# Kernel tuning notes

Hardware: AMD Instinct MI355X
Metric: run time of the kernel (lower is better)

Reference implementation:

```python
import jax, jax.numpy as jnp
import numpy as np

EPS = 1e-5

def _ln(x, g, b):
    m = jnp.mean(x, axis=-1, keepdims=True)
    v = jnp.var(x, axis=-1, keepdims=True)
    return (x - m) / jnp.sqrt(v + EPS) * g + b

def _lin(x, w, b):
    # torch-style weight [out, in]
    return x @ w.T + b

def _mlp(x, w1, b1, w2, b2):
    # Mlp: Linear -> exact GELU -> Linear (dropout=0)
    return _lin(jax.nn.gelu(_lin(x, w1, b1), approximate=False), w2, b2)

def setup_inputs() -> dict:
    B, C, H, W = 2, 256, 64, 64
    key = jax.random.key(0)
    ks = jax.random.split(key, 32)
    s = 0.02  # param init scale keeps attention logits in a sane range
    d = {
        'center_fea': jax.random.normal(ks[0], (B, C, H, W), jnp.float32),
        'wh_fea':     jax.random.normal(ks[1], (B, C, H, W), jnp.float32),
        'cls_fea':    jax.random.normal(ks[2], (B, C, H, W), jnp.float32),
        'mix_w': jax.random.normal(ks[3], (C, 3 * C), jnp.float32) * s,
        'mix_b': jnp.zeros((C,), jnp.float32),
        'ln_g': jnp.ones((C,), jnp.float32),
        'ln_b': jnp.zeros((C,), jnp.float32),
        'q1_w': jax.random.normal(ks[4], (C, C), jnp.float32) * s,
        'q1_b': jnp.zeros((C,), jnp.float32),
        'q2_w': jax.random.normal(ks[5], (C, C), jnp.float32) * s,
        'q2_b': jnp.zeros((C,), jnp.float32),
        'q3_w': jax.random.normal(ks[6], (C, C), jnp.float32) * s,
        'q3_b': jnp.zeros((C,), jnp.float32),
        'k_w': jax.random.normal(ks[7], (C, C), jnp.float32) * s,
        'k_b': jnp.zeros((C,), jnp.float32),
        'v_w': jax.random.normal(ks[8], (C, C), jnp.float32) * s,
        'v_b': jnp.zeros((C,), jnp.float32),
        'cmlp_w1': jax.random.normal(ks[9], (C, C), jnp.float32) * s,
        'cmlp_b1': jnp.zeros((C,), jnp.float32),
        'cmlp_w2': jax.random.normal(ks[10], (C, C), jnp.float32) * s,
        'cmlp_b2': jnp.zeros((C,), jnp.float32),
        'wmlp_w1': jax.random.normal(ks[11], (C, C), jnp.float32) * s,
        'wmlp_b1': jnp.zeros((C,), jnp.float32),
        'wmlp_w2': jax.random.normal(ks[12], (C, C), jnp.float32) * s,
        'wmlp_b2': jnp.zeros((C,), jnp.float32),
        'clsmlp_w1': jax.random.normal(ks[13], (C, C), jnp.float32) * s,
        'clsmlp_b1': jnp.zeros((C,), jnp.float32),
        'clsmlp_w2': jax.random.normal(ks[14], (C, C), jnp.float32) * s,
        'clsmlp_b2': jnp.zeros((C,), jnp.float32),
    }
    return d

def reference(center_fea, wh_fea, cls_fea, mix_w, mix_b, ln_g, ln_b,
              q1_w, q1_b, q2_w, q2_b, q3_w, q3_b, k_w, k_b, v_w, v_b,
              cmlp_w1, cmlp_b1, cmlp_w2, cmlp_b2,
              wmlp_w1, wmlp_b1, wmlp_w2, wmlp_b2,
              clsmlp_w1, clsmlp_b1, clsmlp_w2, clsmlp_b2):
    b, c, h, w = center_fea.shape
    # 1x1 conv mix over concatenated channels [b, 3c, h, w] -> [b, c, h, w]
    cat = jnp.concatenate([center_fea, wh_fea, cls_fea], axis=1)
    mix = jnp.einsum('oc,bchw->bohw', mix_w, cat) + mix_b[None, :, None, None]

    tok = lambda x: x.reshape(b, c, h * w).transpose(0, 2, 1)  # [b, N, c]
    cf, wf, clf, mf = tok(center_fea), tok(wh_fea), tok(cls_fea), tok(mix)

    ct, wt, clt, mt = _ln(cf, ln_g, ln_b), _ln(wf, ln_g, ln_b), _ln(clf, ln_g, ln_b), _ln(mf, ln_g, ln_b)

    kf = _lin(mt, k_w, k_b)  # shared K
    vf = _lin(mt, v_w, v_b)  # shared V

    def attend(q):
        score = jax.nn.softmax(jnp.einsum('bnd,bmd->bnm', q, kf), axis=-1)  # [b, N, N]
        return jnp.einsum('bnm,bmd->bnd', score, vf)

    cf  = _ln(cf  + attend(_lin(ct,  q1_w, q1_b)), ln_g, ln_b)
    wf  = _ln(wf  + attend(_lin(wt,  q2_w, q2_b)), ln_g, ln_b)
    clf = _ln(clf + attend(_lin(clt, q3_w, q3_b)), ln_g, ln_b)

    cf  = _ln(cf  + _mlp(cf,  cmlp_w1, cmlp_b1, cmlp_w2, cmlp_b2), ln_g, ln_b)
    wf  = _ln(wf  + _mlp(wf,  wmlp_w1, wmlp_b1, wmlp_w2, wmlp_b2), ln_g, ln_b)
    clf = _ln(clf + _mlp(clf, clsmlp_w1, clsmlp_b1, clsmlp_w2, clsmlp_b2), ln_g, ln_b)

    untok = lambda x: x.transpose(0, 2, 1).reshape(b, c, h, w)
    return (untok(cf), untok(wf), untok(clf))
```

## Files before the change

kernel.cpp:

```cpp
#include <hip/hip_runtime.h>
#include <hip/hip_bf16.h>
#include <math.h>

typedef unsigned int   u32;
typedef unsigned short u16;
typedef float floatx4 __attribute__((ext_vector_type(4)));
typedef short bf16x8  __attribute__((ext_vector_type(8)));

#define MFMA16(a,b,c) __builtin_amdgcn_mfma_f32_16x16x32_bf16((a),(b),(c),0,0,0)

static __device__ __forceinline__ float bfbits2f(u16 h){
    return __uint_as_float(((u32)h) << 16);
}
static __device__ __forceinline__ u16 f2bfbits(float f){
    u32 u = __float_as_uint(f);
    u32 r = (u + 0x7fffu + ((u >> 16) & 1u)) >> 16;
    return (u16)r;
}
static __device__ __forceinline__ bool sniff_bf16(const void* ln_g){
    return ((const u32*)ln_g)[0] == 0x3f803f80u;
}

typedef __attribute__((address_space(1))) const unsigned int gas_u32;
typedef __attribute__((address_space(3))) unsigned int las_u32;
static __device__ __forceinline__ void gl_lds16(const void* g, void* l){
    __builtin_amdgcn_global_load_lds((gas_u32*)g, (las_u32*)l, 16, 0, 0);
}

#define DPPF(v, ctrl) __uint_as_float((u32)__builtin_amdgcn_update_dpp( \
        (int)__float_as_uint(v), (int)__float_as_uint(v), (ctrl), 0xf, 0xf, true))

static __device__ __forceinline__ float red16_max(float v){
    v = fmaxf(v, DPPF(v, 0xB1));
    v = fmaxf(v, DPPF(v, 0x4E));
    v = fmaxf(v, DPPF(v, 0x141));
    v = fmaxf(v, DPPF(v, 0x140));
    return v;
}
static __device__ __forceinline__ float red16_sum(float v){
    v += DPPF(v, 0xB1);
    v += DPPF(v, 0x4E);
    v += DPPF(v, 0x141);
    v += DPPF(v, 0x140);
    return v;
}

struct PackJob { const void* src; void* dst; int n; int mode; };
struct PackParams { PackJob jobs[26]; const void* lng; };

__global__ __launch_bounds__(256) void k_pack(PackParams p){
    bool isb = sniff_bf16(p.lng);
    PackJob j = p.jobs[blockIdx.y];
    for (int i = blockIdx.x * 256 + threadIdx.x; i < j.n; i += 256 * 256){
        float v = isb ? bfbits2f(((const u16*)j.src)[i]) : ((const float*)j.src)[i];
        if (j.mode == 0) ((u16*)j.dst)[i]  = f2bfbits(v);
        else             ((float*)j.dst)[i] = v;
    }
}

struct FtParams { const void* src[3]; u16* dst[3]; const void* lng; };

__global__ __launch_bounds__(256) void k_feat_t(FtParams p){
    bool isb = sniff_bf16(p.lng);
    int z = blockIdx.z; int si = z >> 1; int b = z & 1;
    const void* src = p.src[si]; u16* dst = p.dst[si];
    int n0 = blockIdx.x * 64, c0 = blockIdx.y * 64;
    __shared__ float tile[64][65];
    int t = threadIdx.x; int tx = t & 63; int ty = t >> 6;
    #pragma unroll
    for (int pp = 0; pp < 16; ++pp){
        int cl = ty + pp * 4;
        size_t off = ((size_t)b * 256 + c0 + cl) * 4096 + n0 + tx;
        float v = isb ? bfbits2f(((const u16*)src)[off]) : ((const float*)src)[off];
        tile[cl][tx] = v;
    }
    __syncthreads();
    #pragma unroll
    for (int pp = 0; pp < 16; ++pp){
        int nl = ty + pp * 4; int cl = tx;
        dst[((size_t)b * 4096 + n0 + nl) * 256 + c0 + cl] = f2bfbits(tile[cl][nl]);
    }
}

struct GemmJob { const u16* A0; const u16* A1; const u16* A2;
                 const u16* W; const float* bias; const u16* res; u16* out; };
struct GemmParams { GemmJob jobs[5]; int K; int op; };

__global__ __launch_bounds__(256, 4) void k_gemm(GemmParams p){
    GemmJob j = p.jobs[blockIdx.z];
    int m0 = blockIdx.x * 64, n0 = blockIdx.y * 64;
    __shared__ __align__(16) u16 As[2][64][64];
    __shared__ __align__(16) u16 Bs[2][64][64];
    int t = threadIdx.x;
    int wave = t >> 6, lane = t & 63, l15 = lane & 15, quad = lane >> 4;
    int mh = (wave & 1) * 32, nh = (wave >> 1) * 32;
    int key = l15 & 7;

    auto stage = [&](int bi, int k0){
        const u16* Ap = (k0 < 256) ? j.A0 : (k0 < 512 ? j.A1 : j.A2);
        int koff = k0 & 255;
        #pragma unroll
        for (int i = 0; i < 2; ++i){
            int rq = wave * 2 + i;
            int r  = rq * 8 + (lane >> 3);
            int gs = (lane & 7) ^ (r & 7);
            gl_lds16(Ap  + (size_t)(m0 + r) * 256 + koff + gs * 8, &As[bi][rq * 8][0]);
            gl_lds16(j.W + (size_t)(n0 + r) * p.K + k0   + gs * 8, &Bs[bi][rq * 8][0]);
        }
    };

    floatx4 acc[2][2];
    #pragma unroll
    for (int a = 0; a < 2; ++a)
        #pragma unroll
        for (int bq = 0; bq < 2; ++bq) acc[a][bq] = (floatx4){0.f,0.f,0.f,0.f};

    stage(0, 0);
    __syncthreads();
    int nk = p.K >> 6, buf = 0;

    for (int ks = 0; ks < nk; ++ks){
        if (ks + 1 < nk) stage(buf ^ 1, (ks + 1) * 64);
        #pragma unroll
        for (int kc = 0; kc < 2; ++kc){
            int gsel = ((kc * 4 + quad) ^ key) * 8;
            bf16x8 a0 = *(const bf16x8*)&As[buf][mh +      l15][gsel];
            bf16x8 a1 = *(const bf16x8*)&As[buf][mh + 16 + l15][gsel];
            bf16x8 b0 = *(const bf16x8*)&Bs[buf][nh +      l15][gsel];
            bf16x8 b1 = *(const bf16x8*)&Bs[buf][nh + 16 + l15][gsel];
            acc[0][0] = MFMA16(a0, b0, acc[0][0]);
            acc[0][1] = MFMA16(a0, b1, acc[0][1]);
            acc[1][0] = MFMA16(a1, b0, acc[1][0]);
            acc[1][1] = MFMA16(a1, b1, acc[1][1]);
        }
        __syncthreads();
        buf ^= 1;
    }

    #pragma unroll
    for (int mb = 0; mb < 2; ++mb)
        #pragma unroll
        for (int nb = 0; nb < 2; ++nb){
            int col = n0 + nh + nb * 16 + l15;
            float bias = j.bias[col];
            #pragma unroll
            for (int rg = 0; rg < 4; ++rg){
                int row = m0 + mh + mb * 16 + quad * 4 + rg;
                float v = acc[mb][nb][rg] + bias;
                if (p.op == 1)      v = 0.5f * v * (1.0f + erff(v * 0.70710678118f));
                else if (p.op == 2) v += bfbits2f(j.res[(size_t)row * 256 + col]);
                j.out[(size_t)row * 256 + col] = f2bfbits(v);
            }
        }
}

struct LnJob { const u16* src; u16* dst; };
struct LnParams { LnJob jobs[4]; const float* g; const float* b; };

__global__ __launch_bounds__(256, 4) void k_ln(LnParams p){
    LnJob j = p.jobs[blockIdx.y];
    int g16 = threadIdx.x >> 4, l = threadIdx.x & 15;
    size_t tok = (size_t)blockIdx.x * 16 + g16;
    const u16* row = j.src + tok * 256 + l * 16;
    uint4 ra = *(const uint4*)(row);
    uint4 rb = *(const uint4*)(row + 8);
    u32 wv[8] = {ra.x, ra.y, ra.z, ra.w, rb.x, rb.y, rb.z, rb.w};
    float va[16];
    float s1 = 0.f, s2 = 0.f;
    #pragma unroll
    for (int i = 0; i < 8; ++i){
        float a = bfbits2f((u16)(wv[i] & 0xffffu));
        float c = bfbits2f((u16)(wv[i] >> 16));
        va[2*i] = a; va[2*i+1] = c;
        s1 += a + c; s2 += a*a + c*c;
    }
    s1 = red16_sum(s1); s2 = red16_sum(s2);
    float mean = s1 * (1.f/256.f);
    float var  = s2 * (1.f/256.f) - mean * mean;
    float rstd = rsqrtf(var + 1e-5f);
    int c0 = l * 16;
    u32 ow[8];
    #pragma unroll
    for (int i = 0; i < 8; ++i){
        float x0 = (va[2*i]   - mean) * rstd * p.g[c0 + 2*i]     + p.b[c0 + 2*i];
        float x1 = (va[2*i+1] - mean) * rstd * p.g[c0 + 2*i + 1] + p.b[c0 + 2*i + 1];
        ow[i] = (u32)f2bfbits(x0) | ((u32)f2bfbits(x1) << 16);
    }
    u16* dst = j.dst + tok * 256 + c0;
    *(uint4*)(dst)     = (uint4){ow[0], ow[1], ow[2], ow[3]};
    *(uint4*)(dst + 8) = (uint4){ow[4], ow[5], ow[6], ow[7]};
}

__global__ __launch_bounds__(256, 4) void k_vt(const u16* __restrict__ Vf, u16* __restrict__ Vt){
    int b = blockIdx.z;
    int n0 = blockIdx.x * 64, c0 = blockIdx.y * 64;
    __shared__ u16 tile[64][66];
    int t = threadIdx.x; int tx = t & 63; int ty = t >> 6;
    #pragma unroll
    for (int pp = 0; pp < 16; ++pp){
        int nl = ty + pp * 4;
        tile[nl][tx] = Vf[((size_t)b * 4096 + n0 + nl) * 256 + c0 + tx];
    }
    __syncthreads();
    #pragma unroll
    for (int pp = 0; pp < 16; ++pp){
        int cl = ty + pp * 4; int nl = tx;
        Vt[((size_t)b * 256 + c0 + cl) * 4096 + n0 + nl] = tile[nl][cl];
    }
}

struct FlashParams {
    const u16* Q[3]; const u16* K; const u16* Vt;
    const u16* Res[3]; u16* Out[3];
    const float* g; const float* b;
};

__global__ __launch_bounds__(256, 2) void k_flash(FlashParams p){
    int s = blockIdx.y >> 1, b = blockIdx.y & 1;
    int m0 = blockIdx.x * 64;
    const u16* Q   = p.Q[s]   + (size_t)b * 4096 * 256;
    const u16* Kf  = p.K      + (size_t)b * 4096 * 256;
    const u16* Vtg = p.Vt     + (size_t)b * 256 * 4096;
    const u16* Res = p.Res[s] + (size_t)b * 4096 * 256;
    u16*       Out = p.Out[s] + (size_t)b * 4096 * 256;

    __shared__ __align__(16) u16 Kb[2][32][256];
    __shared__ __align__(16) u16 Vb[2][256][32];
    __shared__ __align__(16) u16 Pl[4][16][40];

    int t = threadIdx.x, wave = t >> 6, lane = t & 63, l15 = lane & 15, quad = lane >> 4;

    auto stage = [&](int bi, int kv0){
        #pragma unroll
        for (int m = 0; m < 4; ++m){
            int q = wave * 4 + m;
            int r0 = q * 2 + (lane >> 5);
            int gg = (lane & 31) ^ (r0 & 7);
            gl_lds16(Kf + (size_t)(kv0 + r0) * 256 + gg * 8, &Kb[bi][q * 2][0]);
        }
        #pragma unroll
        for (int m = 0; m < 4; ++m){
            int q = wave * 4 + m;
            int d = q * 16 + (lane >> 2);
            int gg = (lane & 3) ^ ((d >> 1) & 3);
            gl_lds16(Vtg + (size_t)d * 4096 + kv0 + gg * 8, &Vb[bi][q * 16][0]);
        }
    };

    stage(0, 0);

    bf16x8 qf[8];
    {
        const u16* qrow = Q + (size_t)(m0 + wave * 16 + l15) * 256 + quad * 8;
        #pragma unroll
        for (int kc = 0; kc < 8; ++kc) qf[kc] = *(const bf16x8*)(qrow + kc * 32);
    }
    floatx4 o[16];
    #pragma unroll
    for (int i = 0; i < 16; ++i) o[i] = (floatx4){0.f,0.f,0.f,0.f};
    float mrow[4] = {-INFINITY,-INFINITY,-INFINITY,-INFINITY};
    float lsum[4] = {0.f,0.f,0.f,0.f};

    __syncthreads();
    int buf = 0;

    for (int ch = 0; ch < 128; ++ch){
        if (ch < 127) stage(buf ^ 1, (ch + 1) * 32);

        floatx4 sa[2];
        __builtin_amdgcn_s_setprio(1);
        #pragma unroll
        for (int sub = 0; sub < 2; ++sub){
            int row = sub * 16 + l15;
            floatx4 a0 = (floatx4){0.f,0.f,0.f,0.f};
            floatx4 a1 = (floatx4){0.f,0.f,0.f,0.f};
            #pragma unroll
            for (int kc = 0; kc < 4; ++kc){
                bf16x8 kb0 = *(const bf16x8*)&Kb[buf][row][((((2*kc  ) * 4 + quad) ^ (row & 7))) * 8];
                bf16x8 kb1 = *(const bf16x8*)&Kb[buf][row][((((2*kc+1) * 4 + quad) ^ (row & 7))) * 8];
                a0 = MFMA16(qf[2*kc  ], kb0, a0);
                a1 = MFMA16(qf[2*kc+1], kb1, a1);
            }
            sa[sub] = a0 + a1;
        }
        __builtin_amdgcn_s_setprio(0);

        float al[4]; int grow = 0;
        #pragma unroll
        for (int rg = 0; rg < 4; ++rg){
            float m1 = red16_max(fmaxf(sa[0][rg], sa[1][rg]));
            grow |= (m1 > mrow[rg]) ? 1 : 0;
            float mn = fmaxf(mrow[rg], m1);
            al[rg] = __expf(mrow[rg] - mn);
            mrow[rg] = mn;
        }
        #pragma unroll
        for (int rg = 0; rg < 4; ++rg){
            float p0 = __expf(sa[0][rg] - mrow[rg]);
            float p1 = __expf(sa[1][rg] - mrow[rg]);
            sa[0][rg] = p0; sa[1][rg] = p1;
            lsum[rg] = lsum[rg] * al[rg] + (p0 + p1);
        }

        #pragma unroll
        for (int sub = 0; sub < 2; ++sub)
            #pragma unroll
            for (int rg = 0; rg < 4; ++rg)
                Pl[wave][quad * 4 + rg][sub * 16 + l15] = f2bfbits(sa[sub][rg]);

        if (__any(grow)){
            #pragma unroll
            for (int dc = 0; dc < 16; ++dc)
                #pragma unroll
                for (int rg = 0; rg < 4; ++rg) o[dc][rg] *= al[rg];
        }

        asm volatile("s_waitcnt lgkmcnt(0)" ::: "memory");
        __builtin_amdgcn_sched_barrier(0);

        bf16x8 pa = *(const bf16x8*)&Pl[wave][l15][quad * 8];
        __builtin_amdgcn_s_setprio(1);
        #pragma unroll
        for (int dc = 0; dc < 16; ++dc){
            int row = dc * 16 + l15;
            bf16x8 vb = *(const bf16x8*)&Vb[buf][row][((quad ^ ((row >> 1) & 3))) * 8];
            o[dc] = MFMA16(pa, vb, o[dc]);
        }
        __builtin_amdgcn_s_setprio(0);

        __syncthreads();
        buf ^= 1;
    }

    float inv[4];
    #pragma unroll
    for (int rg = 0; rg < 4; ++rg) inv[rg] = 1.0f / red16_sum(lsum[rg]);
    float s1[4] = {0.f,0.f,0.f,0.f}, s2[4] = {0.f,0.f,0.f,0.f};
    #pragma unroll
    for (int dc = 0; dc < 16; ++dc)
        #pragma unroll
        for (int rg = 0; rg < 4; ++rg){
            int row = m0 + wave * 16 + quad * 4 + rg;
            float v = o[dc][rg] * inv[rg] + bfbits2f(Res[(size_t)row * 256 + dc * 16 + l15]);
            o[dc][rg] = v;
            s1[rg] += v; s2[rg] += v * v;
        }
    #pragma unroll
    for (int rg = 0; rg < 4; ++rg){
        float mean = red16_sum(s1[rg]) * (1.f/256.f);
        float q2   = red16_sum(s2[rg]);
        float var  = q2 * (1.f/256.f) - mean * mean;
        s1[rg] = mean; s2[rg] = rsqrtf(var + 1e-5f);
    }
    #pragma unroll
    for (int dc = 0; dc < 16; ++dc){
        int c = dc * 16 + l15;
        float gv = p.g[c], bv = p.b[c];
        #pragma unroll
        for (int rg = 0; rg < 4; ++rg){
            int row = m0 + wave * 16 + quad * 4 + rg;
            Out[(size_t)row * 256 + c] = f2bfbits((o[dc][rg] - s1[rg]) * s2[rg] * gv + bv);
        }
    }
}

struct OutTParams { const u16* F[3]; void* out; const void* lng; };

__global__ __launch_bounds__(256, 4) void k_out_t(OutTParams p){
    bool isb = sniff_bf16(p.lng);
    int z = blockIdx.z; int s = z >> 1; int b = z & 1;
    const u16* F = p.F[s];
    int n0 = blockIdx.x * 64, c0 = blockIdx.y * 64;
    __shared__ u16 tile[64][66];
    int t = threadIdx.x; int tx = t & 63; int ty = t >> 6;
    #pragma unroll
    for (int pp = 0; pp < 16; ++pp){
        int nl = ty + pp * 4;
        tile[nl][tx] = F[((size_t)b * 4096 + n0 + nl) * 256 + c0 + tx];
    }
    __syncthreads();
    size_t obase = ((size_t)s * 2 + b) * 256 * 4096;
    #pragma unroll
    for (int pp = 0; pp < 16; ++pp){
        int cl = ty + pp * 4; int nl = tx;
        u16 raw = tile[nl][cl];
        size_t off = obase + (size_t)(c0 + cl) * 4096 + n0 + nl;
        if (isb) ((u16*)p.out)[off]   = raw;
        else     ((float*)p.out)[off] = bfbits2f(raw);
    }
}

extern "C" void kernel_launch(void* const* d_in, const int* in_sizes, int n_in,
                              void* d_out, int out_size, void* d_ws, size_t ws_size,
                              hipStream_t stream) {
    (void)in_sizes; (void)n_in; (void)out_size; (void)ws_size;
    const size_t SLOT = (size_t)2 * 4096 * 256;
    u16* ws = (u16*)d_ws;
    auto slot = [&](int i){ return ws + (size_t)i * SLOT; };

    u16 *Tc = slot(0),  *Tw = slot(1),  *Tcl = slot(2),  *Tm = slot(3);
    u16 *Lc = slot(4),  *Lw = slot(5),  *Lcl = slot(6),  *Lm = slot(7);
    u16 *Q1 = slot(8),  *Q2 = slot(9),  *Q3  = slot(10);
    u16 *Kf = slot(11), *Vf = slot(12), *Vt  = slot(13);
    u16 *Yc = slot(14), *Yw = slot(15), *Ycl = slot(16);
    u16 *Hc = Q1, *Hw = Q2, *Hcl = Q3;
    u16 *Zc = Lc, *Zw = Lw, *Zcl = Lcl;
    u16 *Fc = Kf, *Fw = Vf, *Fcl = Vt;

    u16* wbase = slot(17);
    u16 *mixw = wbase;
    u16 *q1w = wbase + 196608, *q2w = q1w + 65536, *q3w = q2w + 65536;
    u16 *kw  = q3w + 65536,    *vw  = kw  + 65536;
    u16 *cw1 = vw  + 65536, *cw2 = cw1 + 65536, *ww1 = cw2 + 65536,
        *ww2 = ww1 + 65536, *clw1 = ww2 + 65536, *clw2 = clw1 + 65536;
    float* pbase = (float*)(wbase + 1048576);
    float *mixb = pbase,        *lng = pbase+256,  *lnb = pbase+512,
          *q1b = pbase+768,  *q2b = pbase+1024, *q3b = pbase+1280,
          *kb  = pbase+1536, *vb  = pbase+1792,
          *cb1 = pbase+2048, *cb2 = pbase+2304, *wb1 = pbase+2560,
          *wb2 = pbase+2816, *clb1= pbase+3072, *clb2= pbase+3328;

    {
        PackParams pp;
        const int widx[12] = {3,7,9,11,13,15,17,19,21,23,25,27};
        u16* wdst[12] = {mixw,q1w,q2w,q3w,kw,vw,cw1,cw2,ww1,ww2,clw1,clw2};
        for (int i = 0; i < 12; ++i)
            pp.jobs[i] = PackJob{ d_in[widx[i]], wdst[i], (i==0?196608:65536), 0 };
        const int pidx[14] = {4,5,6,8,10,12,14,16,18,20,22,24,26,28};
        float* pdst[14] = {mixb,lng,lnb,q1b,q2b,q3b,kb,vb,cb1,cb2,wb1,wb2,clb1,clb2};
        for (int i = 0; i < 14; ++i)
            pp.jobs[12+i] = PackJob{ d_in[pidx[i]], pdst[i], 256, 1 };
        pp.lng = d_in[5];
        hipLaunchKernelGGL(k_pack, dim3(256, 26), dim3(256), 0, stream, pp);
    }
    {
        FtParams fp;
        fp.src[0] = d_in[0]; fp.src[1] = d_in[1]; fp.src[2] = d_in[2];
        fp.dst[0] = Tc; fp.dst[1] = Tw; fp.dst[2] = Tcl;
        fp.lng = d_in[5];
        hipLaunchKernelGGL(k_feat_t, dim3(64, 4, 6), dim3(256), 0, stream, fp);
    }
    {
        GemmParams gp; gp.K = 768; gp.op = 0;
        gp.jobs[0] = GemmJob{ Tc, Tw, Tcl, mixw, mixb, nullptr, Tm };
        hipLaunchKernelGGL(k_gemm, dim3(128, 4, 1), dim3(256), 0, stream, gp);
    }
    {
        LnParams lp; lp.g = lng; lp.b = lnb;
        lp.jobs[0] = LnJob{Tc, Lc}; lp.jobs[1] = LnJob{Tw, Lw};
        lp.jobs[2] = LnJob{Tcl, Lcl}; lp.jobs[3] = LnJob{Tm, Lm};
        hipLaunchKernelGGL(k_ln, dim3(512, 4), dim3(256), 0, stream, lp);
    }
    {
        GemmParams gp; gp.K = 256; gp.op = 0;
        gp.jobs[0] = GemmJob{ Lc,  nullptr, nullptr, q1w, q1b, nullptr, Q1 };
        gp.jobs[1] = GemmJob{ Lw,  nullptr, nullptr, q2w, q2b, nullptr, Q2 };
        gp.jobs[2] = GemmJob{ Lcl, nullptr, nullptr, q3w, q3b, nullptr, Q3 };
        gp.jobs[3] = GemmJob{ Lm,  nullptr, nullptr, kw,  kb,  nullptr, Kf };
        gp.jobs[4] = GemmJob{ Lm,  nullptr, nullptr, vw,  vb,  nullptr, Vf };
        hipLaunchKernelGGL(k_gemm, dim3(128, 4, 5), dim3(256), 0, stream, gp);
    }
    hipLaunchKernelGGL(k_vt, dim3(64, 4, 2), dim3(256), 0, stream, Vf, Vt);
    {
        FlashParams fp;
        fp.Q[0] = Q1; fp.Q[1] = Q2; fp.Q[2] = Q3;
        fp.K = Kf; fp.Vt = Vt;
        fp.Res[0] = Tc; fp.Res[1] = Tw; fp.Res[2] = Tcl;
        fp.Out[0] = Yc; fp.Out[1] = Yw; fp.Out[2] = Ycl;
        fp.g = lng; fp.b = lnb;
        hipLaunchKernelGGL(k_flash, dim3(64, 6), dim3(256), 0, stream, fp);
    }
    {
        GemmParams gp; gp.K = 256; gp.op = 1;
        gp.jobs[0] = GemmJob{ Yc,  nullptr, nullptr, cw1,  cb1,  nullptr, Hc };
        gp.jobs[1] = GemmJob{ Yw,  nullptr, nullptr, ww1,  wb1,  nullptr, Hw };
        gp.jobs[2] = GemmJob{ Ycl, nullptr, nullptr, clw1, clb1, nullptr, Hcl };
        hipLaunchKernelGGL(k_gemm, dim3(128, 4, 3), dim3(256), 0, stream, gp);
    }
    {
        GemmParams gp; gp.K = 256; gp.op = 2;
        gp.jobs[0] = GemmJob{ Hc,  nullptr, nullptr, cw2,  cb2,  Yc,  Zc };
        gp.jobs[1] = GemmJob{ Hw,  nullptr, nullptr, ww2,  wb2,  Yw,  Zw };
        gp.jobs[2] = GemmJob{ Hcl, nullptr, nullptr, clw2, clb2, Ycl, Zcl };
        hipLaunchKernelGGL(k_gemm, dim3(128, 4, 3), dim3(256), 0, stream, gp);
    }
    {
        LnParams lp; lp.g = lng; lp.b = lnb;
        lp.jobs[0] = LnJob{Zc, Fc}; lp.jobs[1] = LnJob{Zw, Fw};
        lp.jobs[2] = LnJob{Zcl, Fcl}; lp.jobs[3] = LnJob{Zc, Fc};
        hipLaunchKernelGGL(k_ln, dim3(512, 3), dim3(256), 0, stream, lp);
    }
    {
        OutTParams op;
        op.F[0] = Fc; op.F[1] = Fw; op.F[2] = Fcl;
        op.out = d_out; op.lng = d_in[5];
        hipLaunchKernelGGL(k_out_t, dim3(64, 4, 6), dim3(256), 0, stream, op);
    }
}
```

Measured before the change: 426.2 us.

## Fuse final LayerNorm with output transpose, template GEMM on BM, drop setprio

```diff
diff --git a/kernel.cpp b/kernel.cpp
--- a/kernel.cpp
+++ b/kernel.cpp
@@ -86,32 +86,42 @@
                  const u16* W; const float* bias; const u16* res; u16* out; };
 struct GemmParams { GemmJob jobs[5]; int K; int op; };
 
-__global__ __launch_bounds__(256, 4) void k_gemm(GemmParams p){
+template<int BM>
+__global__ __launch_bounds__(256, (BM == 64) ? 4 : 3) void k_gemm(GemmParams p){
+    constexpr int MW = BM / 2;
+    constexpr int MB = MW / 16;
+    constexpr int AI = BM / 32;
     GemmJob j = p.jobs[blockIdx.z];
-    int m0 = blockIdx.x * 64, n0 = blockIdx.y * 64;
-    __shared__ __align__(16) u16 As[2][64][64];
+    int m0 = blockIdx.x * BM, n0 = blockIdx.y * 64;
+    __shared__ __align__(16) u16 As[2][BM][64];
     __shared__ __align__(16) u16 Bs[2][64][64];
     int t = threadIdx.x;
     int wave = t >> 6, lane = t & 63, l15 = lane & 15, quad = lane >> 4;
-    int mh = (wave & 1) * 32, nh = (wave >> 1) * 32;
+    int mh = (wave & 1) * MW, nh = (wave >> 1) * 32;
     int key = l15 & 7;
 
     auto stage = [&](int bi, int k0){
         const u16* Ap = (k0 < 256) ? j.A0 : (k0 < 512 ? j.A1 : j.A2);
         int koff = k0 & 255;
+        #pragma unroll
+        for (int i = 0; i < AI; ++i){
+            int rq = wave * AI + i;
+            int r  = rq * 8 + (lane >> 3);
+            int gs = (lane & 7) ^ (r & 7);
+            gl_lds16(Ap + (size_t)(m0 + r) * 256 + koff + gs * 8, &As[bi][rq * 8][0]);
+        }
         #pragma unroll
         for (int i = 0; i < 2; ++i){
             int rq = wave * 2 + i;
             int r  = rq * 8 + (lane >> 3);
             int gs = (lane & 7) ^ (r & 7);
-            gl_lds16(Ap  + (size_t)(m0 + r) * 256 + koff + gs * 8, &As[bi][rq * 8][0]);
-            gl_lds16(j.W + (size_t)(n0 + r) * p.K + k0   + gs * 8, &Bs[bi][rq * 8][0]);
+            gl_lds16(j.W + (size_t)(n0 + r) * p.K + k0 + gs * 8, &Bs[bi][rq * 8][0]);
         }
     };
 
-    floatx4 acc[2][2];
-    #pragma unroll
-    for (int a = 0; a < 2; ++a)
+    floatx4 acc[MB][2];
+    #pragma unroll
+    for (int a = 0; a < MB; ++a)
         #pragma unroll
         for (int bq = 0; bq < 2; ++bq) acc[a][bq] = (floatx4){0.f,0.f,0.f,0.f};
 
@@ -124,21 +134,24 @@
         #pragma unroll
         for (int kc = 0; kc < 2; ++kc){
             int gsel = ((kc * 4 + quad) ^ key) * 8;
-            bf16x8 a0 = *(const bf16x8*)&As[buf][mh +      l15][gsel];
-            bf16x8 a1 = *(const bf16x8*)&As[buf][mh + 16 + l15][gsel];
-            bf16x8 b0 = *(const bf16x8*)&Bs[buf][nh +      l15][gsel];
-            bf16x8 b1 = *(const bf16x8*)&Bs[buf][nh + 16 + l15][gsel];
-            acc[0][0] = MFMA16(a0, b0, acc[0][0]);
-            acc[0][1] = MFMA16(a0, b1, acc[0][1]);
-            acc[1][0] = MFMA16(a1, b0, acc[1][0]);
-            acc[1][1] = MFMA16(a1, b1, acc[1][1]);
+            bf16x8 av[MB], bv[2];
+            #pragma unroll
+            for (int mb = 0; mb < MB; ++mb)
+                av[mb] = *(const bf16x8*)&As[buf][mh + mb * 16 + l15][gsel];
+            bv[0] = *(const bf16x8*)&Bs[buf][nh +      l15][gsel];
+            bv[1] = *(const bf16x8*)&Bs[buf][nh + 16 + l15][gsel];
+            #pragma unroll
+            for (int mb = 0; mb < MB; ++mb){
+                acc[mb][0] = MFMA16(av[mb], bv[0], acc[mb][0]);
+                acc[mb][1] = MFMA16(av[mb], bv[1], acc[mb][1]);
+            }
         }
         __syncthreads();
         buf ^= 1;
     }
 
     #pragma unroll
-    for (int mb = 0; mb < 2; ++mb)
+    for (int mb = 0; mb < MB; ++mb)
         #pragma unroll
         for (int nb = 0; nb < 2; ++nb){
             int col = n0 + nh + nb * 16 + l15;
@@ -191,6 +204,57 @@
     *(uint4*)(dst + 8) = (uint4){ow[4], ow[5], ow[6], ow[7]};
 }
 
+struct LnOutParams { const u16* Z[3]; void* out; const float* g; const float* b; const void* lng; };
+
+__global__ __launch_bounds__(256, 4) void k_ln_out(LnOutParams p){
+    bool isb = sniff_bf16(p.lng);
+    int y = blockIdx.y; int s = y >> 1, b = y & 1;
+    const u16* Z = p.Z[s] + (size_t)b * 4096 * 256;
+    int tok0 = blockIdx.x * 64;
+    __shared__ u16 tile[64][258];
+    int t = threadIdx.x, g16 = t >> 4, l = t & 15;
+    #pragma unroll
+    for (int pass = 0; pass < 4; ++pass){
+        int tl = pass * 16 + g16;
+        const u16* row = Z + (size_t)(tok0 + tl) * 256 + l * 16;
+        uint4 ra = *(const uint4*)(row);
+        uint4 rb = *(const uint4*)(row + 8);
+        u32 wv[8] = {ra.x, ra.y, ra.z, ra.w, rb.x, rb.y, rb.z, rb.w};
+        float va[16];
+        float s1 = 0.f, s2 = 0.f;
+        #pragma unroll
+        for (int i = 0; i < 8; ++i){
+            float a = bfbits2f((u16)(wv[i] & 0xffffu));
+            float c = bfbits2f((u16)(wv[i] >> 16));
+            va[2*i] = a; va[2*i+1] = c;
+            s1 += a + c; s2 += a*a + c*c;
+        }
+        s1 = red16_sum(s1); s2 = red16_sum(s2);
+        float mean = s1 * (1.f/256.f);
+        float var  = s2 * (1.f/256.f) - mean * mean;
+        float rstd = rsqrtf(var + 1e-5f);
+        int c0 = l * 16;
+        u32* drow = (u32*)&tile[tl][c0];
+        #pragma unroll
+        for (int i = 0; i < 8; ++i){
+            float x0 = (va[2*i]   - mean) * rstd * p.g[c0 + 2*i]     + p.b[c0 + 2*i];
+            float x1 = (va[2*i+1] - mean) * rstd * p.g[c0 + 2*i + 1] + p.b[c0 + 2*i + 1];
+            drow[i] = (u32)f2bfbits(x0) | ((u32)f2bfbits(x1) << 16);
+        }
+    }
+    __syncthreads();
+    size_t obase = ((size_t)s * 2 + b) * 256 * 4096;
+    int cq = t >> 6, tl2 = t & 63;
+    #pragma unroll
+    for (int pp = 0; pp < 64; ++pp){
+        int c = pp * 4 + cq;
+        u16 raw = tile[tl2][c];
+        size_t off = obase + (size_t)c * 4096 + tok0 + tl2;
+        if (isb) ((u16*)p.out)[off]   = raw;
+        else     ((float*)p.out)[off] = bfbits2f(raw);
+    }
+}
+
 __global__ __launch_bounds__(256, 4) void k_vt(const u16* __restrict__ Vf, u16* __restrict__ Vt){
     int b = blockIdx.z;
     int n0 = blockIdx.x * 64, c0 = blockIdx.y * 64;
@@ -268,7 +332,6 @@
         if (ch < 127) stage(buf ^ 1, (ch + 1) * 32);
 
         floatx4 sa[2];
-        __builtin_amdgcn_s_setprio(1);
         #pragma unroll
         for (int sub = 0; sub < 2; ++sub){
             int row = sub * 16 + l15;
@@ -283,7 +346,6 @@
             }
             sa[sub] = a0 + a1;
         }
-        __builtin_amdgcn_s_setprio(0);
 
         float al[4]; int grow = 0;
         #pragma unroll
@@ -319,14 +381,12 @@
         __builtin_amdgcn_sched_barrier(0);
 
         bf16x8 pa = *(const bf16x8*)&Pl[wave][l15][quad * 8];
-        __builtin_amdgcn_s_setprio(1);
         #pragma unroll
         for (int dc = 0; dc < 16; ++dc){
             int row = dc * 16 + l15;
             bf16x8 vb = *(const bf16x8*)&Vb[buf][row][((quad ^ ((row >> 1) & 3))) * 8];
             o[dc] = MFMA16(pa, vb, o[dc]);
         }
-        __builtin_amdgcn_s_setprio(0);
 
         __syncthreads();
         buf ^= 1;
@@ -361,32 +421,6 @@
             int row = m0 + wave * 16 + quad * 4 + rg;
             Out[(size_t)row * 256 + c] = f2bfbits((o[dc][rg] - s1[rg]) * s2[rg] * gv + bv);
         }
-    }
-}
-
-struct OutTParams { const u16* F[3]; void* out; const void* lng; };
-
-__global__ __launch_bounds__(256, 4) void k_out_t(OutTParams p){
-    bool isb = sniff_bf16(p.lng);
-    int z = blockIdx.z; int s = z >> 1; int b = z & 1;
-    const u16* F = p.F[s];
-    int n0 = blockIdx.x * 64, c0 = blockIdx.y * 64;
-    __shared__ u16 tile[64][66];
-    int t = threadIdx.x; int tx = t & 63; int ty = t >> 6;
-    #pragma unroll
-    for (int pp = 0; pp < 16; ++pp){
-        int nl = ty + pp * 4;
-        tile[nl][tx] = F[((size_t)b * 4096 + n0 + nl) * 256 + c0 + tx];
-    }
-    __syncthreads();
-    size_t obase = ((size_t)s * 2 + b) * 256 * 4096;
-    #pragma unroll
-    for (int pp = 0; pp < 16; ++pp){
-        int cl = ty + pp * 4; int nl = tx;
-        u16 raw = tile[nl][cl];
-        size_t off = obase + (size_t)(c0 + cl) * 4096 + n0 + nl;
-        if (isb) ((u16*)p.out)[off]   = raw;
-        else     ((float*)p.out)[off] = bfbits2f(raw);
     }
 }
 
@@ -405,7 +439,6 @@
     u16 *Yc = slot(14), *Yw = slot(15), *Ycl = slot(16);
     u16 *Hc = Q1, *Hw = Q2, *Hcl = Q3;
     u16 *Zc = Lc, *Zw = Lw, *Zcl = Lcl;
-    u16 *Fc = Kf, *Fw = Vf, *Fcl = Vt;
 
     u16* wbase = slot(17);
     u16 *mixw = wbase;
@@ -443,7 +476,7 @@
     {
         GemmParams gp; gp.K = 768; gp.op = 0;
         gp.jobs[0] = GemmJob{ Tc, Tw, Tcl, mixw, mixb, nullptr, Tm };
-        hipLaunchKernelGGL(k_gemm, dim3(128, 4, 1), dim3(256), 0, stream, gp);
+        hipLaunchKernelGGL((k_gemm<64>), dim3(128, 4, 1), dim3(256), 0, stream, gp);
     }
     {
         LnParams lp; lp.g = lng; lp.b = lnb;
@@ -458,7 +491,7 @@
         gp.jobs[2] = GemmJob{ Lcl, nullptr, nullptr, q3w, q3b, nullptr, Q3 };
         gp.jobs[3] = GemmJob{ Lm,  nullptr, nullptr, kw,  kb,  nullptr, Kf };
         gp.jobs[4] = GemmJob{ Lm,  nullptr, nullptr, vw,  vb,  nullptr, Vf };
-        hipLaunchKernelGGL(k_gemm, dim3(128, 4, 5), dim3(256), 0, stream, gp);
+        hipLaunchKernelGGL((k_gemm<128>), dim3(64, 4, 5), dim3(256), 0, stream, gp);
     }
     hipLaunchKernelGGL(k_vt, dim3(64, 4, 2), dim3(256), 0, stream, Vf, Vt);
     {
@@ -475,25 +508,19 @@
         gp.jobs[0] = GemmJob{ Yc,  nullptr, nullptr, cw1,  cb1,  nullptr, Hc };
         gp.jobs[1] = GemmJob{ Yw,  nullptr, nullptr, ww1,  wb1,  nullptr, Hw };
         gp.jobs[2] = GemmJob{ Ycl, nullptr, nullptr, clw1, clb1, nullptr, Hcl };
-        hipLaunchKernelGGL(k_gemm, dim3(128, 4, 3), dim3(256), 0, stream, gp);
+        hipLaunchKernelGGL((k_gemm<128>), dim3(64, 4, 3), dim3(256), 0, stream, gp);
     }
     {
         GemmParams gp; gp.K = 256; gp.op = 2;
         gp.jobs[0] = GemmJob{ Hc,  nullptr, nullptr, cw2,  cb2,  Yc,  Zc };
         gp.jobs[1] = GemmJob{ Hw,  nullptr, nullptr, ww2,  wb2,  Yw,  Zw };
         gp.jobs[2] = GemmJob{ Hcl, nullptr, nullptr, clw2, clb2, Ycl, Zcl };
-        hipLaunchKernelGGL(k_gemm, dim3(128, 4, 3), dim3(256), 0, stream, gp);
-    }
-    {
-        LnParams lp; lp.g = lng; lp.b = lnb;
-        lp.jobs[0] = LnJob{Zc, Fc}; lp.jobs[1] = LnJob{Zw, Fw};
-        lp.jobs[2] = LnJob{Zcl, Fcl}; lp.jobs[3] = LnJob{Zc, Fc};
-        hipLaunchKernelGGL(k_ln, dim3(512, 3), dim3(256), 0, stream, lp);
-    }
-    {
-        OutTParams op;
-        op.F[0] = Fc; op.F[1] = Fw; op.F[2] = Fcl;
-        op.out = d_out; op.lng = d_in[5];
-        hipLaunchKernelGGL(k_out_t, dim3(64, 4, 6), dim3(256), 0, stream, op);
-    }
-}
+        hipLaunchKernelGGL((k_gemm<128>), dim3(64, 4, 3), dim3(256), 0, stream, gp);
+    }
+    {
+        LnOutParams lo;
+        lo.Z[0] = Zc; lo.Z[1] = Zw; lo.Z[2] = Zcl;
+        lo.out = d_out; lo.g = lng; lo.b = lnb; lo.lng = d_in[5];
+        hipLaunchKernelGGL(k_ln_out, dim3(64, 6), dim3(256), 0, stream, lo);
+    }
+}
```

Result: no change. 427.6 us (+0.3%).
